# Optimization experiments

Measured on AMD Instinct MI355X. Metric: run time of the kernel, lower is better.

## Reference

```python
import jax, jax.numpy as jnp
import numpy as np

DIM = 768
HEADS = 6
POINTS = 4
HIDDEN = 192
EPS = 1e-6
B = 4
HQ = WQ = HKV = WKV = 64


def layer_norm(x, g, b):
    m = jnp.mean(x, axis=-1, keepdims=True)
    v = jnp.var(x, axis=-1, keepdims=True)
    return (x - m) * jax.lax.rsqrt(v + EPS) * g + b


def ref_points(H, W, dtype):
    # matches torch.linspace(0.5, H-0.5, H)/H grid, stacked as (x, y)
    ry = (jnp.arange(H, dtype=dtype) + 0.5) / H
    rx = (jnp.arange(W, dtype=dtype) + 0.5) / W
    gy, gx = jnp.meshgrid(ry, rx, indexing='ij')
    return jnp.stack([gx.reshape(-1), gy.reshape(-1)], axis=-1)  # (Nq, 2)


def msdeform_attn(query, value_in, ref, H, W, Wo, bo, Wa, ba, Wv, bv, Wp, bp):
    # single-level multi-scale deformable attention (n_levels=1)
    Bq, Nq, D = query.shape
    hd = D // HEADS
    v = (value_in @ Wv + bv).reshape(Bq, H * W, HEADS, hd).transpose(0, 2, 1, 3)  # (B, heads, HW, hd)
    off = (query @ Wo + bo).reshape(Bq, Nq, HEADS, POINTS, 2)
    aw = jax.nn.softmax((query @ Wa + ba).reshape(Bq, Nq, HEADS, POINTS), axis=-1)
    loc = ref[None, :, None, None, :] + off / jnp.array([W, H], dtype=query.dtype)  # normalized [0,1]
    # grid_sample align_corners=False pixel coords, zero padding
    x = loc[..., 0] * W - 0.5
    y = loc[..., 1] * H - 0.5
    x0 = jnp.floor(x)
    y0 = jnp.floor(y)
    wx = x - x0
    wy = y - y0

    def gather(xi, yi):
        xi_i = xi.astype(jnp.int32)
        yi_i = yi.astype(jnp.int32)
        valid = (xi_i >= 0) & (xi_i < W) & (yi_i >= 0) & (yi_i < H)
        idx = jnp.clip(yi_i, 0, H - 1) * W + jnp.clip(xi_i, 0, W - 1)  # (B, Nq, heads, P)
        idx_t = idx.transpose(0, 2, 1, 3).reshape(Bq, HEADS, Nq * POINTS, 1)
        g = jnp.take_along_axis(v, idx_t, axis=2).reshape(Bq, HEADS, Nq, POINTS, hd)
        return g * valid.transpose(0, 2, 1, 3)[..., None]

    def bw(w):  # (B, Nq, heads, P) -> (B, heads, Nq, P, 1)
        return w.transpose(0, 2, 1, 3)[..., None]

    s = (gather(x0, y0) * bw((1 - wx) * (1 - wy))
         + gather(x0 + 1, y0) * bw(wx * (1 - wy))
         + gather(x0, y0 + 1) * bw((1 - wx) * wy)
         + gather(x0 + 1, y0 + 1) * bw(wx * wy))
    out = jnp.sum(s * bw(aw), axis=3)  # (B, heads, Nq, hd)
    out = out.transpose(0, 2, 1, 3).reshape(Bq, Nq, D)
    return out @ Wp + bp


def conv_ffn(x, H, W, fc1_w, fc1_b, dw_w, dw_b, fc2_w, fc2_b):
    Bq, N, _ = x.shape
    h = x @ fc1_w + fc1_b  # (B, N, HIDDEN)
    hm = h.reshape(Bq, H, W, HIDDEN).transpose(0, 3, 1, 2)
    hm = jax.lax.conv_general_dilated(hm, dw_w, (1, 1), 'SAME',
                                      feature_group_count=HIDDEN,
                                      dimension_numbers=('NCHW', 'OIHW', 'NCHW'))
    hm = hm + dw_b[None, :, None, None]
    h = hm.transpose(0, 2, 3, 1).reshape(Bq, N, HIDDEN)
    h = jax.nn.gelu(h, approximate=False)
    return h @ fc2_w + fc2_b


def setup_inputs() -> dict:
    key = jax.random.key(0)
    ks = jax.random.split(key, 20)
    d = {}
    d['c'] = jax.random.normal(ks[0], (B, HQ * WQ, DIM), jnp.float32)
    d['x_vit'] = jax.random.normal(ks[1], (B, HKV * WKV, DIM), jnp.float32)
    d['y_vit'] = jax.random.normal(ks[2], (B, HKV * WKV, DIM), jnp.float32)
    for nm in ['qn', 'fnx', 'fny', 'fn']:
        d[nm + '_g'] = jnp.ones((DIM,), jnp.float32)
        d[nm + '_b'] = jnp.zeros((DIM,), jnp.float32)
    i = 3
    for p in ['x', 'y']:
        d[p + 'o_w'] = jax.random.normal(ks[i], (DIM, HEADS * POINTS * 2), jnp.float32) * 0.02; i += 1
        d[p + 'o_b'] = jax.random.normal(ks[i], (HEADS * POINTS * 2,), jnp.float32) * 0.1; i += 1
        d[p + 'a_w'] = jax.random.normal(ks[i], (DIM, HEADS * POINTS), jnp.float32) * 0.02; i += 1
        d[p + 'a_b'] = jnp.zeros((HEADS * POINTS,), jnp.float32)
        d[p + 'v_w'] = jax.random.normal(ks[i], (DIM, DIM), jnp.float32) * 0.02; i += 1
        d[p + 'v_b'] = jnp.zeros((DIM,), jnp.float32)
        d[p + 'p_w'] = jax.random.normal(ks[i], (DIM, DIM), jnp.float32) * 0.02; i += 1
        d[p + 'p_b'] = jnp.zeros((DIM,), jnp.float32)
    d['gate_x'] = jnp.full((1,), 0.5, jnp.float32)
    d['gate_y'] = jnp.full((1,), 0.5, jnp.float32)
    d['fc1_w'] = jax.random.normal(ks[13], (DIM, HIDDEN), jnp.float32) * 0.02
    d['fc1_b'] = jnp.zeros((HIDDEN,), jnp.float32)
    d['dw_w'] = jax.random.normal(ks[14], (HIDDEN, 1, 3, 3), jnp.float32) * 0.1
    d['dw_b'] = jnp.zeros((HIDDEN,), jnp.float32)
    d['fc2_w'] = jax.random.normal(ks[15], (HIDDEN, DIM), jnp.float32) * 0.02
    d['fc2_b'] = jnp.zeros((DIM,), jnp.float32)
    d['H_q'] = HQ
    d['W_q'] = WQ
    d['H_kv'] = HKV
    d['W_kv'] = WKV
    return d


def reference(c, x_vit, y_vit, qn_g, qn_b, fnx_g, fnx_b, fny_g, fny_b,
              xo_w, xo_b, xa_w, xa_b, xv_w, xv_b, xp_w, xp_b,
              yo_w, yo_b, ya_w, ya_b, yv_w, yv_b, yp_w, yp_b,
              gate_x, gate_y, fn_g, fn_b,
              fc1_w, fc1_b, dw_w, dw_b, fc2_w, fc2_b,
              H_q, W_q, H_kv, W_kv):
    ref = ref_points(H_q, W_q, c.dtype)
    query = layer_norm(c, qn_g, qn_b)
    upd_x = msdeform_attn(query, layer_norm(x_vit, fnx_g, fnx_b), ref, H_kv, W_kv,
                          xo_w, xo_b, xa_w, xa_b, xv_w, xv_b, xp_w, xp_b)
    upd_y = msdeform_attn(query, layer_norm(y_vit, fny_g, fny_b), ref, H_kv, W_kv,
                          yo_w, yo_b, ya_w, ya_b, yv_w, yv_b, yp_w, yp_b)
    c_mid = c + gate_x * upd_x + gate_y * upd_y
    c_final = c_mid + conv_ffn(layer_norm(c_mid, fn_g, fn_b), H_q, W_q,
                               fc1_w, fc1_b, dw_w, dw_b, fc2_w, fc2_b)
    return c_final
```

## Files before the change

kernel.cpp:

```cpp
#include <hip/hip_runtime.h>
#include <hip/hip_bf16.h>
#include <hip/hip_fp16.h>
#include <math.h>

using bf16 = __hip_bfloat16;

#define DIM 768
#define HEADS 6
#define HD 128
#define NPTS 4
#define HIDDEN 192
#define BQ 4
#define HQ 64
#define WQ 64
#define NQ (HQ * WQ)
#define MROWS (BQ * NQ)

typedef __attribute__((ext_vector_type(8))) short bf16x8;
typedef __attribute__((ext_vector_type(4))) float f32x4;

__device__ __forceinline__ float b2f(bf16 x) { return __bfloat162float(x); }
__device__ __forceinline__ bf16 f2b(float x) { return __float2bfloat16(x); }
__device__ __forceinline__ float bru(unsigned short u) {
    return __uint_as_float(((unsigned)u) << 16);
}
__device__ __forceinline__ unsigned short f2bu(float v) {
    bf16 t = __float2bfloat16(v);
    return *reinterpret_cast<unsigned short*>(&t);
}
__device__ __forceinline__ float ldT(const void* p, size_t i, int f32) {
    return f32 ? ((const float*)p)[i] : b2f(((const bf16*)p)[i]);
}
__device__ __forceinline__ void stT(void* p, size_t i, int f32, float v) {
    if (f32) ((float*)p)[i] = v; else ((bf16*)p)[i] = f2b(v);
}

__global__ void detect_kernel(const unsigned* __restrict__ w, int* __restrict__ flag) {
    *flag = (w[0] == 0x3F800000u) ? 1 : 0;
}

__global__ void __launch_bounds__(256)
transpose_kernel(const void* __restrict__ W, bf16* __restrict__ Wt,
                 int K, int N, const int* __restrict__ dtf) {
    const int f32 = *dtf;
    __shared__ float t[32][33];
    const int tx = threadIdx.x & 31, ty = threadIdx.x >> 5;
    const int kb = blockIdx.y * 32, nb = blockIdx.x * 32;
#pragma unroll
    for (int i = 0; i < 4; i++) {
        const int k = kb + ty + i * 8;
        t[ty + i * 8][tx] = ldT(W, (size_t)k * N + nb + tx, f32);
    }
    __syncthreads();
#pragma unroll
    for (int i = 0; i < 4; i++) {
        const int n = nb + ty + i * 8;
        Wt[(size_t)n * K + kb + tx] = f2b(t[tx][ty + i * 8]);
    }
}

__global__ void __launch_bounds__(256)
pack_bt_small_kernel(const void* __restrict__ Wo, const void* __restrict__ Wa,
                     bf16* __restrict__ Bt, const int* __restrict__ dtf) {
    const int f32 = *dtf;
    const int idx = blockIdx.x * 256 + threadIdx.x;
    const int n = idx / DIM, k = idx % DIM;
    float v = 0.f;
    if (n < 48) v = ldT(Wo, (size_t)k * 48 + n, f32);
    else if (n < 72) v = ldT(Wa, (size_t)k * 24 + (n - 48), f32);
    Bt[idx] = f2b(v);
}

__global__ void pack_bias_small_kernel(const void* __restrict__ bo,
                                       const void* __restrict__ ba,
                                       float* __restrict__ out,
                                       const int* __restrict__ dtf) {
    const int f32 = *dtf;
    const int t = threadIdx.x;
    float v = 0.f;
    if (t < 48) v = ldT(bo, t, f32);
    else if (t < 72) v = ldT(ba, t - 48, f32);
    out[t] = v;
}

__global__ void __launch_bounds__(256)
stats768_kernel(const void* __restrict__ x, float* __restrict__ stats,
                const int* __restrict__ dtf) {
    const int f32 = *dtf;
    const int row = blockIdx.x;
    const int tid = threadIdx.x;
    const size_t base = (size_t)row * DIM;
    float v[3];
#pragma unroll
    for (int i = 0; i < 3; i++) v[i] = ldT(x, base + tid + i * 256, f32);
    float s = v[0] + v[1] + v[2];
    float sq = v[0] * v[0] + v[1] * v[1] + v[2] * v[2];
#pragma unroll
    for (int o = 32; o > 0; o >>= 1) {
        s += __shfl_down(s, o);
        sq += __shfl_down(sq, o);
    }
    __shared__ float ss[4], sqs[4];
    const int wave = tid >> 6, lane = tid & 63;
    if (lane == 0) { ss[wave] = s; sqs[wave] = sq; }
    __syncthreads();
    if (tid == 0) {
        const float ts = ss[0] + ss[1] + ss[2] + ss[3];
        const float tq = sqs[0] + sqs[1] + sqs[2] + sqs[3];
        const float mean = ts * (1.0f / DIM);
        const float var = tq * (1.0f / DIM) - mean * mean;
        stats[(size_t)row * 2 + 0] = mean;
        stats[(size_t)row * 2 + 1] = rsqrtf(var + 1e-6f);
    }
}

enum { EPI_BF16 = 0, EPI_F32 = 1, EPI_GATE_INIT = 2, EPI_GATE_ACC = 3,
       EPI_FINAL = 4, EPI_SMALL = 5 };

template <int EPI, bool LNA>
__global__ void __launch_bounds__(256, 2)
gemm_mfma_kernel(const void* __restrict__ Av, size_t row0, size_t crow0,
                 const float* __restrict__ stats,
                 const void* __restrict__ ga, const void* __restrict__ be,
                 const bf16* __restrict__ Bt, const void* __restrict__ bias,
                 bf16* __restrict__ outI, float* __restrict__ outF,
                 __half* __restrict__ oh1, __half* __restrict__ oh2,
                 const void* __restrict__ resid, void* __restrict__ cmid,
                 const void* __restrict__ gate,
                 int N, int K, const int* __restrict__ dtf) {
    constexpr int BM = 64, BN = 64, BK = 32;
    constexpr int NI = 4;
    constexpr int LK = BK + 8;

    __shared__ short As[2][BM][LK];
    __shared__ short Bs[2][BN][LK];
    __shared__ float gS[LNA ? DIM : 1];
    __shared__ float bS[LNA ? DIM : 1];

    const int f32 = *dtf;
    const int tid = threadIdx.x;
    const int m0 = blockIdx.y * BM;
    const int n0 = blockIdx.x * BN;
    const int w = tid >> 6, lane = tid & 63;
    const int lm = lane & 15, lq = lane >> 4;
    const int sar = tid >> 2, sak = (tid & 3) * 8;
    const size_t arow = row0 + m0 + sar;

    float amean = 0.f, arstd = 0.f;
    if (LNA) {
        amean = stats[arow * 2];
        arstd = stats[arow * 2 + 1];
        for (int j = tid; j < DIM; j += 256) {
            gS[j] = ldT(ga, j, f32);
            bS[j] = ldT(be, j, f32);
        }
    }

    int4 rA0[2], rA1[2], rB0[1], rB1[1];

    auto loadT = [&](int k0, int4* ra, int4* rb) {
        if (LNA && f32) {
            const int4* ap = (const int4*)((const float*)Av + arow * (size_t)K + (k0 + sak));
            ra[0] = ap[0]; ra[1] = ap[1];
        } else {
            const int4* ap = (const int4*)((const bf16*)Av + arow * (size_t)K + (k0 + sak));
            ra[0] = ap[0];
        }
        rb[0] = *(const int4*)(Bt + (size_t)(n0 + sar) * K + (k0 + sak));
    };

    auto storeT = [&](int k0, const int4* ra, const int4* rb, int buf) {
        if (LNA) {
            float av[8];
            if (f32) {
#pragma unroll
                for (int j = 0; j < 2; j++)
#pragma unroll
                    for (int e = 0; e < 4; e++)
                        av[4 * j + e] = __int_as_float(((const int*)&ra[j])[e]);
            } else {
#pragma unroll
                for (int e = 0; e < 4; e++) {
                    const unsigned ua = ((const unsigned*)&ra[0])[e];
                    av[2 * e + 0] = bru((unsigned short)(ua & 0xffffu));
                    av[2 * e + 1] = bru((unsigned short)(ua >> 16));
                }
            }
            unsigned p[4];
#pragma unroll
            for (int i = 0; i < 4; i++) {
                const int kk = k0 + sak + 2 * i;
                const float v0 = (av[2 * i + 0] - amean) * arstd * gS[kk + 0] + bS[kk + 0];
                const float v1 = (av[2 * i + 1] - amean) * arstd * gS[kk + 1] + bS[kk + 1];
                p[i] = (unsigned)f2bu(v0) | ((unsigned)f2bu(v1) << 16);
            }
            *(int4*)&As[buf][sar][sak] = make_int4(p[0], p[1], p[2], p[3]);
        } else {
            *(int4*)&As[buf][sar][sak] = ra[0];
        }
        *(int4*)&Bs[buf][sar][sak] = rb[0];
    };

    f32x4 acc[NI];
#pragma unroll
    for (int ni = 0; ni < NI; ni++) acc[ni] = (f32x4){0.f, 0.f, 0.f, 0.f};

    auto computeT = [&](int buf) {
        const bf16x8 af = *(const bf16x8*)&As[buf][w * 16 + lm][lq * 8];
        bf16x8 bfr[NI];
#pragma unroll
        for (int ni = 0; ni < NI; ni++)
            bfr[ni] = *(const bf16x8*)&Bs[buf][ni * 16 + lm][lq * 8];
#pragma unroll
        for (int ni = 0; ni < NI; ni++)
            acc[ni] = __builtin_amdgcn_mfma_f32_16x16x32_bf16(af, bfr[ni], acc[ni], 0, 0, 0);
    };

    const int NT = K / BK;
    loadT(0, rA0, rB0);
    __syncthreads();
    storeT(0, rA0, rB0, 0);
    loadT(BK, rA1, rB1);
    __syncthreads();
    for (int tt = 0; tt < NT; tt += 2) {
        if (tt + 2 < NT) loadT((tt + 2) * BK, rA0, rB0);
        computeT(0);
        storeT((tt + 1) * BK, rA1, rB1, 1);
        __syncthreads();
        if (tt + 3 < NT) loadT((tt + 3) * BK, rA1, rB1);
        computeT(1);
        if (tt + 2 < NT) storeT((tt + 2) * BK, rA0, rB0, 0);
        __syncthreads();
    }

    float gf = 0.f;
    if (EPI == EPI_GATE_INIT || EPI == EPI_GATE_ACC) gf = ldT(gate, 0, f32);
#pragma unroll
    for (int ni = 0; ni < NI; ni++) {
        const int col = n0 + ni * 16 + lm;
        const float bv = (EPI == EPI_SMALL) ? ((const float*)bias)[col]
                                            : ldT(bias, col, f32);
        const f32x4 a = acc[ni];
#pragma unroll
        for (int r = 0; r < 4; r++) {
            const int lrow = m0 + w * 16 + lq * 4 + r;
            const float v = a[r] + bv;
            if (EPI == EPI_BF16) {
                outI[(size_t)lrow * N + col] = f2b(v);
            } else if (EPI == EPI_F32) {
                outF[(size_t)lrow * N + col] = v;
            } else if (EPI == EPI_SMALL) {
                if (col < 48) oh1[(size_t)lrow * 48 + col] = __float2half(v);
                else if (col < 72) oh2[(size_t)lrow * 24 + (col - 48)] = __float2half(v);
            } else if (EPI == EPI_GATE_INIT) {
                const size_t od = (crow0 + lrow) * (size_t)DIM + col;
                stT(cmid, od, f32, ldT(resid, od, f32) + gf * v);
            } else if (EPI == EPI_GATE_ACC) {
                const size_t od = (crow0 + lrow) * (size_t)DIM + col;
                stT(cmid, od, f32, ldT(cmid, od, f32) + gf * v);
            } else {
                const size_t od = (crow0 + lrow) * (size_t)DIM + col;
                stT(cmid, od, f32, ldT(cmid, od, f32) + v);
            }
        }
    }
}

__global__ void __launch_bounds__(256)
sample_kernel(const bf16* __restrict__ val, const __half* __restrict__ off,
              const __half* __restrict__ aw, bf16* __restrict__ attn,
              size_t m_base) {
    const int g = blockIdx.x * 4 + (threadIdx.x >> 6);
    const int lane = threadIdx.x & 63;
    const int h = g % HEADS;
    const int ml = g / HEADS;
    const size_t m = m_base + ml;
    const int qy = ml >> 6, qx = ml & 63;

    const __half* op = off + m * (HEADS * NPTS * 2) + h * (NPTS * 2);
    const __half* ap = aw + m * (HEADS * NPTS) + h * NPTS;
    const float l0 = __half2float(ap[0]), l1 = __half2float(ap[1]);
    const float l2 = __half2float(ap[2]), l3 = __half2float(ap[3]);
    const float mx = fmaxf(fmaxf(l0, l1), fmaxf(l2, l3));
    float e[4] = {expf(l0 - mx), expf(l1 - mx), expf(l2 - mx), expf(l3 - mx)};
    const float inv = 1.f / (e[0] + e[1] + e[2] + e[3]);

    const float refx = (qx + 0.5f) * (1.0f / WQ);
    const float refy = (qy + 0.5f) * (1.0f / HQ);
    float acc0 = 0.f, acc1 = 0.f;
    const int d0 = h * HD + lane * 2;
    const bf16* vb = val + d0;
#pragma unroll
    for (int p = 0; p < NPTS; p++) {
        const float wp = e[p] * inv;
        const float xx = (refx + __half2float(op[p * 2 + 0]) * (1.0f / 64.f)) * 64.f - 0.5f;
        const float yy = (refy + __half2float(op[p * 2 + 1]) * (1.0f / 64.f)) * 64.f - 0.5f;
        const float x0f = floorf(xx), y0f = floorf(yy);
        const int ix0 = (int)x0f, iy0 = (int)y0f;
        const float wx = xx - x0f, wy = yy - y0f;
        const float cw[4] = {(1.f - wx) * (1.f - wy), wx * (1.f - wy),
                             (1.f - wx) * wy, wx * wy};
#pragma unroll
        for (int ci = 0; ci < 4; ci++) {
            const int ix = ix0 + (ci & 1);
            const int iy = iy0 + (ci >> 1);
            if (ix < 0 || ix >= 64 || iy < 0 || iy >= 64) continue;
            const unsigned u = *(const unsigned*)(vb + ((size_t)((iy << 6) | ix)) * DIM);
            const float ww = wp * cw[ci];
            acc0 = fmaf(ww, bru((unsigned short)(u & 0xffffu)), acc0);
            acc1 = fmaf(ww, bru((unsigned short)(u >> 16)), acc1);
        }
    }
    bf16* o = attn + (size_t)ml * DIM + d0;
    o[0] = f2b(acc0);
    o[1] = f2b(acc1);
}

__global__ void __launch_bounds__(256)
dwconv_gelu_kernel(const float* __restrict__ h1, const void* __restrict__ w,
                   const void* __restrict__ bb, bf16* __restrict__ h2,
                   const int* __restrict__ dtf) {
    const int f32 = *dtf;
    const int idx = blockIdx.x * 256 + threadIdx.x;
    const int TOT = BQ * HQ * WQ * HIDDEN;
    if (idx >= TOT) return;
    const int c = idx % HIDDEN;
    const int x = (idx / HIDDEN) & 63;
    const int y = (idx / (HIDDEN * WQ)) & 63;
    const int b = idx / (HIDDEN * WQ * HQ);
    float acc = ldT(bb, c, f32);
    const float* base = h1 + (size_t)b * NQ * HIDDEN;
#pragma unroll
    for (int ky = 0; ky < 3; ky++) {
        const int yy = y + ky - 1;
        if (yy < 0 || yy >= HQ) continue;
#pragma unroll
        for (int kx = 0; kx < 3; kx++) {
            const int xx = x + kx - 1;
            if (xx < 0 || xx >= WQ) continue;
            acc = fmaf(base[((size_t)(yy * WQ + xx)) * HIDDEN + c],
                       ldT(w, c * 9 + ky * 3 + kx, f32), acc);
        }
    }
    const float gv = 0.5f * acc * (1.0f + erff(acc * 0.70710678118654752f));
    h2[idx] = f2b(gv);
}

extern "C" void kernel_launch(void* const* d_in, const int* in_sizes, int n_in,
                              void* d_out, int out_size, void* d_ws, size_t ws_size,
                              hipStream_t stream) {
    (void)in_sizes; (void)n_in; (void)out_size; (void)ws_size;
    const void* c_in  = d_in[0];
    const void* x_vit = d_in[1];
    const void* y_vit = d_in[2];
    const void* qn_g  = d_in[3];  const void* qn_b  = d_in[4];
    const void* fnx_g = d_in[5];  const void* fnx_b = d_in[6];
    const void* fny_g = d_in[7];  const void* fny_b = d_in[8];
    const void* fn_g  = d_in[9];  const void* fn_b  = d_in[10];
    const void* xo_w = d_in[11];  const void* xo_b = d_in[12];
    const void* xa_w = d_in[13];  const void* xa_b = d_in[14];
    const void* xv_w = d_in[15];  const void* xv_b = d_in[16];
    const void* xp_w = d_in[17];  const void* xp_b = d_in[18];
    const void* yo_w = d_in[19];  const void* yo_b = d_in[20];
    const void* ya_w = d_in[21];  const void* ya_b = d_in[22];
    const void* yv_w = d_in[23];  const void* yv_b = d_in[24];
    const void* yp_w = d_in[25];  const void* yp_b = d_in[26];
    const void* gate_x = d_in[27];
    const void* gate_y = d_in[28];
    const void* fc1_w = d_in[29]; const void* fc1_b = d_in[30];
    const void* dw_w  = d_in[31]; const void* dw_b  = d_in[32];
    const void* fc2_w = d_in[33]; const void* fc2_b = d_in[34];

    char* ws = (char*)d_ws;
    bf16*   fc2T   = (bf16*)(ws + 0);
    bf16*   xvT    = (bf16*)(ws + 294912);
    bf16*   xpT    = (bf16*)(ws + 1474560);
    bf16*   yvT    = (bf16*)(ws + 2654208);
    bf16*   ypT    = (bf16*)(ws + 3833856);
    bf16*   fc1T   = (bf16*)(ws + 5013504);
    __half* offB   = (__half*)(ws + 5308416);
    __half* awB    = (__half*)(ws + 6881280);
    float*  statsQ = (float*)(ws + 7667712);
    float*  statsV = (float*)(ws + 7798784);
    int*    dtf    = (int*)  (ws + 7929856);
    bf16*   val_b  = (bf16*) (ws + 7930112);
    bf16*   attn_b = (bf16*) (ws + 14221568);
    bf16*   btS    = (bf16*) (ws + 20513024);
    float*  biasS  = (float*)(ws + 20709632);
    float*  h1     = (float*)(ws + 7930112);
    bf16*   h2     = (bf16*) (ws + 294912);
    void*   cmid   = d_out;

    const dim3 gB(12, 64);
    const dim3 gF(12, 256);
    const dim3 gFc1(3, 256);
    const dim3 gSmall(2, 256);

    detect_kernel<<<1, 1, 0, stream>>>((const unsigned*)qn_g, dtf);

    transpose_kernel<<<dim3(24, 24), 256, 0, stream>>>(xv_w, xvT, DIM, DIM, dtf);
    transpose_kernel<<<dim3(24, 24), 256, 0, stream>>>(xp_w, xpT, DIM, DIM, dtf);
    transpose_kernel<<<dim3(24, 24), 256, 0, stream>>>(yv_w, yvT, DIM, DIM, dtf);
    transpose_kernel<<<dim3(24, 24), 256, 0, stream>>>(yp_w, ypT, DIM, DIM, dtf);
    transpose_kernel<<<dim3(6, 24), 256, 0, stream>>>(fc1_w, fc1T, DIM, HIDDEN, dtf);
    transpose_kernel<<<dim3(24, 6), 256, 0, stream>>>(fc2_w, fc2T, HIDDEN, DIM, dtf);

    stats768_kernel<<<MROWS, 256, 0, stream>>>(c_in, statsQ, dtf);

    pack_bt_small_kernel<<<384, 256, 0, stream>>>(xo_w, xa_w, btS, dtf);
    pack_bias_small_kernel<<<1, 128, 0, stream>>>(xo_b, xa_b, biasS, dtf);
    gemm_mfma_kernel<EPI_SMALL, true><<<gSmall, 256, 0, stream>>>(
        c_in, 0, 0, statsQ, qn_g, qn_b, btS, biasS, nullptr, nullptr,
        offB, awB, nullptr, nullptr, nullptr, 128, DIM, dtf);
    stats768_kernel<<<MROWS, 256, 0, stream>>>(x_vit, statsV, dtf);
    for (int b = 0; b < BQ; b++) {
        const size_t r0 = (size_t)b * NQ;
        gemm_mfma_kernel<EPI_BF16, true><<<gB, 256, 0, stream>>>(
            x_vit, r0, 0, statsV, fnx_g, fnx_b, xvT, xv_b, val_b, nullptr,
            nullptr, nullptr, nullptr, nullptr, nullptr, DIM, DIM, dtf);
        sample_kernel<<<NQ * HEADS / 4, 256, 0, stream>>>(val_b, offB, awB, attn_b, r0);
        gemm_mfma_kernel<EPI_GATE_INIT, false><<<gB, 256, 0, stream>>>(
            attn_b, 0, r0, nullptr, nullptr, nullptr, xpT, xp_b, nullptr, nullptr,
            nullptr, nullptr, c_in, cmid, gate_x, DIM, DIM, dtf);
    }

    pack_bt_small_kernel<<<384, 256, 0, stream>>>(yo_w, ya_w, btS, dtf);
    pack_bias_small_kernel<<<1, 128, 0, stream>>>(yo_b, ya_b, biasS, dtf);
    gemm_mfma_kernel<EPI_SMALL, true><<<gSmall, 256, 0, stream>>>(
        c_in, 0, 0, statsQ, qn_g, qn_b, btS, biasS, nullptr, nullptr,
        offB, awB, nullptr, nullptr, nullptr, 128, DIM, dtf);
    stats768_kernel<<<MROWS, 256, 0, stream>>>(y_vit, statsV, dtf);
    for (int b = 0; b < BQ; b++) {
        const size_t r0 = (size_t)b * NQ;
        gemm_mfma_kernel<EPI_BF16, true><<<gB, 256, 0, stream>>>(
            y_vit, r0, 0, statsV, fny_g, fny_b, yvT, yv_b, val_b, nullptr,
            nullptr, nullptr, nullptr, nullptr, nullptr, DIM, DIM, dtf);
        sample_kernel<<<NQ * HEADS / 4, 256, 0, stream>>>(val_b, offB, awB, attn_b, r0);
        gemm_mfma_kernel<EPI_GATE_ACC, false><<<gB, 256, 0, stream>>>(
            attn_b, 0, r0, nullptr, nullptr, nullptr, ypT, yp_b, nullptr, nullptr,
            nullptr, nullptr, nullptr, cmid, gate_y, DIM, DIM, dtf);
    }

    stats768_kernel<<<MROWS, 256, 0, stream>>>(cmid, statsQ, dtf);
    gemm_mfma_kernel<EPI_F32, true><<<gFc1, 256, 0, stream>>>(
        cmid, 0, 0, statsQ, fn_g, fn_b, fc1T, fc1_b, nullptr, h1,
        nullptr, nullptr, nullptr, nullptr, nullptr, HIDDEN, DIM, dtf);
    dwconv_gelu_kernel<<<(MROWS * HIDDEN + 255) / 256, 256, 0, stream>>>(h1, dw_w, dw_b, h2, dtf);
    gemm_mfma_kernel<EPI_FINAL, false><<<gF, 256, 0, stream>>>(
        h2, 0, 0, nullptr, nullptr, nullptr, fc2T, fc2_b, nullptr, nullptr,
        nullptr, nullptr, nullptr, cmid, nullptr, DIM, HIDDEN, dtf);
}
```

Before: 1.093 ms.

## Stage GEMM epilogue through LDS for vectorized stores and remap blocks per XCD

The GEMM epilogue now writes the MFMA accumulators into an LDS tile that reuses (via a union) the A/B staging buffers. Each thread then reads 16 contiguous columns and issues vectorized int4/float4 global loads and stores instead of scattered scalar accesses. The grid is flattened to 1D and block indices are remapped so that blocks sharing the same modulo-8 index cover contiguous row bands, aiming to keep related tiles on the same XCD/L2. This adds an extra LDS round-trip and barrier, plus a dependence on grid sizes divisible by 8.

New measurement: 1.257 ms. 1.15x slower.

```diff
diff --git a/kernel.cpp b/kernel.cpp
--- a/kernel.cpp
+++ b/kernel.cpp
@@ -127,20 +127,29 @@
                  __half* __restrict__ oh1, __half* __restrict__ oh2,
                  const void* __restrict__ resid, void* __restrict__ cmid,
                  const void* __restrict__ gate,
-                 int N, int K, const int* __restrict__ dtf) {
+                 int N, int K, int nbx, const int* __restrict__ dtf) {
     constexpr int BM = 64, BN = 64, BK = 32;
     constexpr int NI = 4;
     constexpr int LK = BK + 8;
 
-    __shared__ short As[2][BM][LK];
-    __shared__ short Bs[2][BN][LK];
+    union SMem {
+        struct { short A[2][BM][LK]; short B[2][BN][LK]; } ab;
+        float c[BM][BN + 4];
+    };
+    __shared__ SMem sm;
     __shared__ float gS[LNA ? DIM : 1];
     __shared__ float bS[LNA ? DIM : 1];
 
     const int f32 = *dtf;
     const int tid = threadIdx.x;
-    const int m0 = blockIdx.y * BM;
-    const int n0 = blockIdx.x * BN;
+    const int perx = gridDim.x >> 3;
+    const int c8 = blockIdx.x & 7;
+    const int jj = blockIdx.x >> 3;
+    const int by = c8 * (perx / nbx) + jj / nbx;
+    const int bx = jj % nbx;
+    const int m0 = by * BM;
+    const int n0 = bx * BN;
+
     const int w = tid >> 6, lane = tid & 63;
     const int lm = lane & 15, lq = lane >> 4;
     const int sar = tid >> 2, sak = (tid & 3) * 8;
@@ -194,11 +203,11 @@
                 const float v1 = (av[2 * i + 1] - amean) * arstd * gS[kk + 1] + bS[kk + 1];
                 p[i] = (unsigned)f2bu(v0) | ((unsigned)f2bu(v1) << 16);
             }
-            *(int4*)&As[buf][sar][sak] = make_int4(p[0], p[1], p[2], p[3]);
+            *(int4*)&sm.ab.A[buf][sar][sak] = make_int4(p[0], p[1], p[2], p[3]);
         } else {
-            *(int4*)&As[buf][sar][sak] = ra[0];
-        }
-        *(int4*)&Bs[buf][sar][sak] = rb[0];
+            *(int4*)&sm.ab.A[buf][sar][sak] = ra[0];
+        }
+        *(int4*)&sm.ab.B[buf][sar][sak] = rb[0];
     };
 
     f32x4 acc[NI];
@@ -206,11 +215,11 @@
     for (int ni = 0; ni < NI; ni++) acc[ni] = (f32x4){0.f, 0.f, 0.f, 0.f};
 
     auto computeT = [&](int buf) {
-        const bf16x8 af = *(const bf16x8*)&As[buf][w * 16 + lm][lq * 8];
+        const bf16x8 af = *(const bf16x8*)&sm.ab.A[buf][w * 16 + lm][lq * 8];
         bf16x8 bfr[NI];
 #pragma unroll
         for (int ni = 0; ni < NI; ni++)
-            bfr[ni] = *(const bf16x8*)&Bs[buf][ni * 16 + lm][lq * 8];
+            bfr[ni] = *(const bf16x8*)&sm.ab.B[buf][ni * 16 + lm][lq * 8];
 #pragma unroll
         for (int ni = 0; ni < NI; ni++)
             acc[ni] = __builtin_amdgcn_mfma_f32_16x16x32_bf16(af, bfr[ni], acc[ni], 0, 0, 0);
@@ -237,30 +246,75 @@
     if (EPI == EPI_GATE_INIT || EPI == EPI_GATE_ACC) gf = ldT(gate, 0, f32);
 #pragma unroll
     for (int ni = 0; ni < NI; ni++) {
-        const int col = n0 + ni * 16 + lm;
-        const float bv = (EPI == EPI_SMALL) ? ((const float*)bias)[col]
-                                            : ldT(bias, col, f32);
+        const int ccol = ni * 16 + lm;
         const f32x4 a = acc[ni];
 #pragma unroll
-        for (int r = 0; r < 4; r++) {
-            const int lrow = m0 + w * 16 + lq * 4 + r;
-            const float v = a[r] + bv;
-            if (EPI == EPI_BF16) {
-                outI[(size_t)lrow * N + col] = f2b(v);
-            } else if (EPI == EPI_F32) {
-                outF[(size_t)lrow * N + col] = v;
-            } else if (EPI == EPI_SMALL) {
-                if (col < 48) oh1[(size_t)lrow * 48 + col] = __float2half(v);
-                else if (col < 72) oh2[(size_t)lrow * 24 + (col - 48)] = __float2half(v);
-            } else if (EPI == EPI_GATE_INIT) {
-                const size_t od = (crow0 + lrow) * (size_t)DIM + col;
-                stT(cmid, od, f32, ldT(resid, od, f32) + gf * v);
-            } else if (EPI == EPI_GATE_ACC) {
-                const size_t od = (crow0 + lrow) * (size_t)DIM + col;
-                stT(cmid, od, f32, ldT(cmid, od, f32) + gf * v);
+        for (int r = 0; r < 4; r++)
+            sm.c[w * 16 + lq * 4 + r][ccol] = a[r];
+    }
+    __syncthreads();
+    const int orow = tid >> 2;
+    const int oc0 = (tid & 3) * 16;
+    const int grow = m0 + orow;
+    const int gc0 = n0 + oc0;
+    float vv[16];
+#pragma unroll
+    for (int j = 0; j < 16; j++) vv[j] = sm.c[orow][oc0 + j];
+
+    if (EPI == EPI_SMALL) {
+#pragma unroll
+        for (int j = 0; j < 16; j++) {
+            const int col = gc0 + j;
+            const float v = vv[j] + ((const float*)bias)[col];
+            if (col < 48) oh1[(size_t)grow * 48 + col] = __float2half(v);
+            else if (col < 72) oh2[(size_t)grow * 24 + (col - 48)] = __float2half(v);
+        }
+    } else {
+#pragma unroll
+        for (int j = 0; j < 16; j++) vv[j] += ldT(bias, gc0 + j, f32);
+        if (EPI == EPI_BF16) {
+            unsigned p[8];
+#pragma unroll
+            for (int j = 0; j < 8; j++)
+                p[j] = (unsigned)f2bu(vv[2 * j]) | ((unsigned)f2bu(vv[2 * j + 1]) << 16);
+            int4* dst = (int4*)(outI + (size_t)grow * N + gc0);
+            dst[0] = make_int4(p[0], p[1], p[2], p[3]);
+            dst[1] = make_int4(p[4], p[5], p[6], p[7]);
+        } else if (EPI == EPI_F32) {
+            float* dst = outF + (size_t)grow * N + gc0;
+#pragma unroll
+            for (int j = 0; j < 16; j += 4)
+                *(float4*)(dst + j) = make_float4(vv[j], vv[j + 1], vv[j + 2], vv[j + 3]);
+        } else {
+            const size_t od = (crow0 + grow) * (size_t)DIM + gc0;
+            if (f32) {
+                float* cp = (float*)cmid;
+#pragma unroll
+                for (int j = 0; j < 16; j += 4) {
+                    float4 prev;
+                    if (EPI == EPI_GATE_INIT)
+                        prev = *(const float4*)((const float*)resid + od + j);
+                    else
+                        prev = *(const float4*)(cp + od + j);
+                    float4 o;
+                    if (EPI == EPI_FINAL) {
+                        o.x = prev.x + vv[j];     o.y = prev.y + vv[j + 1];
+                        o.z = prev.z + vv[j + 2]; o.w = prev.w + vv[j + 3];
+                    } else {
+                        o.x = prev.x + gf * vv[j];     o.y = prev.y + gf * vv[j + 1];
+                        o.z = prev.z + gf * vv[j + 2]; o.w = prev.w + gf * vv[j + 3];
+                    }
+                    *(float4*)(cp + od + j) = o;
+                }
             } else {
-                const size_t od = (crow0 + lrow) * (size_t)DIM + col;
-                stT(cmid, od, f32, ldT(cmid, od, f32) + v);
+#pragma unroll
+                for (int j = 0; j < 16; j++) {
+                    float pv;
+                    if (EPI == EPI_GATE_INIT) pv = ldT(resid, od + j, 0);
+                    else pv = ldT(cmid, od + j, 0);
+                    const float o = (EPI == EPI_FINAL) ? (pv + vv[j]) : (pv + gf * vv[j]);
+                    stT(cmid, od + j, 0, o);
+                }
             }
         }
     }
@@ -391,10 +445,10 @@
     bf16*   h2     = (bf16*) (ws + 294912);
     void*   cmid   = d_out;
 
-    const dim3 gB(12, 64);
-    const dim3 gF(12, 256);
-    const dim3 gFc1(3, 256);
-    const dim3 gSmall(2, 256);
+    const int gB = 768,   nbxB = 12;
+    const int gF = 3072,  nbxF = 12;
+    const int gFc1 = 768, nbxFc1 = 3;
+    const int gSm = 512,  nbxSm = 2;
 
     detect_kernel<<<1, 1, 0, stream>>>((const unsigned*)qn_g, dtf);
 
@@ -409,44 +463,44 @@
 
     pack_bt_small_kernel<<<384, 256, 0, stream>>>(xo_w, xa_w, btS, dtf);
     pack_bias_small_kernel<<<1, 128, 0, stream>>>(xo_b, xa_b, biasS, dtf);
-    gemm_mfma_kernel<EPI_SMALL, true><<<gSmall, 256, 0, stream>>>(
+    gemm_mfma_kernel<EPI_SMALL, true><<<gSm, 256, 0, stream>>>(
         c_in, 0, 0, statsQ, qn_g, qn_b, btS, biasS, nullptr, nullptr,
-        offB, awB, nullptr, nullptr, nullptr, 128, DIM, dtf);
+        offB, awB, nullptr, nullptr, nullptr, 128, DIM, nbxSm, dtf);
     stats768_kernel<<<MROWS, 256, 0, stream>>>(x_vit, statsV, dtf);
     for (int b = 0; b < BQ; b++) {
         const size_t r0 = (size_t)b * NQ;
         gemm_mfma_kernel<EPI_BF16, true><<<gB, 256, 0, stream>>>(
             x_vit, r0, 0, statsV, fnx_g, fnx_b, xvT, xv_b, val_b, nullptr,
-            nullptr, nullptr, nullptr, nullptr, nullptr, DIM, DIM, dtf);
+            nullptr, nullptr, nullptr, nullptr, nullptr, DIM, DIM, nbxB, dtf);
         sample_kernel<<<NQ * HEADS / 4, 256, 0, stream>>>(val_b, offB, awB, attn_b, r0);
         gemm_mfma_kernel<EPI_GATE_INIT, false><<<gB, 256, 0, stream>>>(
             attn_b, 0, r0, nullptr, nullptr, nullptr, xpT, xp_b, nullptr, nullptr,
-            nullptr, nullptr, c_in, cmid, gate_x, DIM, DIM, dtf);
+            nullptr, nullptr, c_in, cmid, gate_x, DIM, DIM, nbxB, dtf);
     }
 
     pack_bt_small_kernel<<<384, 256, 0, stream>>>(yo_w, ya_w, btS, dtf);
     pack_bias_small_kernel<<<1, 128, 0, stream>>>(yo_b, ya_b, biasS, dtf);
-    gemm_mfma_kernel<EPI_SMALL, true><<<gSmall, 256, 0, stream>>>(
+    gemm_mfma_kernel<EPI_SMALL, true><<<gSm, 256, 0, stream>>>(
         c_in, 0, 0, statsQ, qn_g, qn_b, btS, biasS, nullptr, nullptr,
-        offB, awB, nullptr, nullptr, nullptr, 128, DIM, dtf);
+        offB, awB, nullptr, nullptr, nullptr, 128, DIM, nbxSm, dtf);
     stats768_kernel<<<MROWS, 256, 0, stream>>>(y_vit, statsV, dtf);
     for (int b = 0; b < BQ; b++) {
         const size_t r0 = (size_t)b * NQ;
         gemm_mfma_kernel<EPI_BF16, true><<<gB, 256, 0, stream>>>(
             y_vit, r0, 0, statsV, fny_g, fny_b, yvT, yv_b, val_b, nullptr,
-            nullptr, nullptr, nullptr, nullptr, nullptr, DIM, DIM, dtf);
+            nullptr, nullptr, nullptr, nullptr, nullptr, DIM, DIM, nbxB, dtf);
         sample_kernel<<<NQ * HEADS / 4, 256, 0, stream>>>(val_b, offB, awB, attn_b, r0);
         gemm_mfma_kernel<EPI_GATE_ACC, false><<<gB, 256, 0, stream>>>(
             attn_b, 0, r0, nullptr, nullptr, nullptr, ypT, yp_b, nullptr, nullptr,
-            nullptr, nullptr, nullptr, cmid, gate_y, DIM, DIM, dtf);
+            nullptr, nullptr, nullptr, cmid, gate_y, DIM, DIM, nbxB, dtf);
     }
 
     stats768_kernel<<<MROWS, 256, 0, stream>>>(cmid, statsQ, dtf);
     gemm_mfma_kernel<EPI_F32, true><<<gFc1, 256, 0, stream>>>(
         cmid, 0, 0, statsQ, fn_g, fn_b, fc1T, fc1_b, nullptr, h1,
-        nullptr, nullptr, nullptr, nullptr, nullptr, HIDDEN, DIM, dtf);
+        nullptr, nullptr, nullptr, nullptr, nullptr, HIDDEN, DIM, nbxFc1, dtf);
     dwconv_gelu_kernel<<<(MROWS * HIDDEN + 255) / 256, 256, 0, stream>>>(h1, dw_w, dw_b, h2, dtf);
     gemm_mfma_kernel<EPI_FINAL, false><<<gF, 256, 0, stream>>>(
         h2, 0, 0, nullptr, nullptr, nullptr, fc2T, fc2_b, nullptr, nullptr,
-        nullptr, nullptr, nullptr, cmid, nullptr, DIM, HIDDEN, dtf);
-}
+        nullptr, nullptr, nullptr, cmid, nullptr, DIM, HIDDEN, nbxF, dtf);
+}
```
